# Optimization experiments

Hardware: AMD Instinct MI355X
Metric: run time of the kernel (lower is better)

Reference implementation:

```python
import jax, jax.numpy as jnp
import numpy as np

N = 50000   # nodes
E = 800000  # edges
D = 128     # input feature dim
HID = 64    # hidden dim
NEG_SLOPE = 0.2


def setup_inputs() -> dict:
    key = jax.random.key(0)
    ks = jax.random.split(key, 12)
    s = 0.1
    x = jax.random.normal(ks[0], (N, D), jnp.float32)
    edge_index = jax.random.randint(ks[1], (2, E), 0, N, dtype=jnp.int64)
    # layer 1: GATConv(128 -> 64, heads=2, concat=False)
    W1 = jax.random.normal(ks[2], (D, 2 * HID), jnp.float32) * s
    a_src1 = jax.random.normal(ks[3], (2, HID), jnp.float32) * s
    a_dst1 = jax.random.normal(ks[4], (2, HID), jnp.float32) * s
    b1 = jnp.zeros((HID,), jnp.float32)
    # layer 2: GATConv(64 -> 64, heads=1, concat=False)
    W2 = jax.random.normal(ks[5], (HID, HID), jnp.float32) * s
    a_src2 = jax.random.normal(ks[6], (1, HID), jnp.float32) * s
    a_dst2 = jax.random.normal(ks[7], (1, HID), jnp.float32) * s
    b2 = jnp.zeros((HID,), jnp.float32)
    # classifier Linear(64 -> 2)
    Wc = jax.random.normal(ks[8], (HID, 2), jnp.float32) * s
    bc = jnp.zeros((2,), jnp.float32)
    return {"x": x, "edge_index": edge_index, "W1": W1, "a_src1": a_src1,
            "a_dst1": a_dst1, "b1": b1, "W2": W2, "a_src2": a_src2,
            "a_dst2": a_dst2, "b2": b2, "Wc": Wc, "bc": bc}


def _gat_layer(x, src, dst, W, a_s, a_d, b, n):
    """PyG GATConv (concat=False -> mean over heads), eval mode."""
    H, C = a_s.shape
    h = (x @ W).reshape(n, H, C)                      # [N,H,C]
    alpha_s = jnp.sum(h * a_s, axis=-1)               # [N,H]
    alpha_d = jnp.sum(h * a_d, axis=-1)               # [N,H]
    e = jax.nn.leaky_relu(alpha_s[src] + alpha_d[dst], NEG_SLOPE)  # [E,H]
    # segment softmax over incoming edges of each target node
    m = jax.ops.segment_max(e, dst, num_segments=n)   # [N,H]
    e = jnp.exp(e - m[dst])
    denom = jax.ops.segment_sum(e, dst, num_segments=n)
    alpha = e / (denom[dst] + 1e-16)                  # [E,H]
    msg = h[src] * alpha[:, :, None]                  # [E,H,C]
    out = jax.ops.segment_sum(msg, dst, num_segments=n)  # [N,H,C]
    return out.mean(axis=1) + b                       # [N,C]


def reference(x, edge_index, W1, a_src1, a_dst1, b1, W2, a_src2, a_dst2, b2, Wc, bc):
    n = x.shape[0]
    loops = jnp.arange(n, dtype=edge_index.dtype)     # PyG add_self_loops=True
    src = jnp.concatenate([edge_index[0], loops])
    dst = jnp.concatenate([edge_index[1], loops])
    h = jax.nn.elu(_gat_layer(x, src, dst, W1, a_src1, a_dst1, b1, n))
    h = jax.nn.elu(_gat_layer(h, src, dst, W2, a_src2, a_dst2, b2, n))
    logits = h @ Wc + bc
    return jax.nn.log_softmax(logits, axis=1)
```

## Files before the change

### kernel.cpp

```cpp
#include <hip/hip_runtime.h>
#include <math.h>

#define NN 50000
#define NE 800000
#define NT (NE + NN)
#define SCAN_BLK 1024
#define NSCAN ((NN + SCAN_BLK - 1) / SCAN_BLK)
#define NBUCK 196
#define BE 4096
#define NBLK_B ((NT + BE - 1) / BE)
#define CAP 6144
#define NBLK_G ((NN + 63) / 64)

typedef short bf16x8 __attribute__((ext_vector_type(8)));
typedef float f32x4 __attribute__((ext_vector_type(4)));
union U16x8 { uint4 u; bf16x8 s; };

__device__ __forceinline__ unsigned pk_bf16x2(float x, float y) {
  unsigned ux = __float_as_uint(x); ux = ux + 0x7FFFu + ((ux >> 16) & 1u);
  unsigned uy = __float_as_uint(y); uy = uy + 0x7FFFu + ((uy >> 16) & 1u);
  return (ux >> 16) | (uy & 0xFFFF0000u);
}
__device__ __forceinline__ unsigned short bf16_1(float x) {
  unsigned u = __float_as_uint(x); u = u + 0x7FFFu + ((u >> 16) & 1u);
  return (unsigned short)(u >> 16);
}
__device__ __forceinline__ float blo(unsigned v) { return __uint_as_float(v << 16); }
__device__ __forceinline__ float bhi(unsigned v) { return __uint_as_float(v & 0xFFFF0000u); }

__global__ __launch_bounds__(256) void k_prep(const float* __restrict__ W1, const float* __restrict__ W2,
                                              unsigned short* __restrict__ w1f,
                                              unsigned short* __restrict__ w2f,
                                              int* __restrict__ deg, int* __restrict__ bcur) {
  int i = blockIdx.x * 256 + threadIdx.x;
  if (i < NN) deg[i] = 0;
  if (i < NBUCK) bcur[i] = i * CAP;
  if (i < 128 * 128) {
    int k = i >> 7, col = i & 127;
    int ct = col >> 4, kt = k >> 5, lane = (((k >> 3) & 3) << 4) | (col & 15), j = k & 7;
    w1f[(((ct << 2) | kt) * 64 + lane) * 8 + j] = bf16_1(W1[i]);
  } else if (i < 128 * 128 + 64 * 64) {
    int e = i - 128 * 128;
    int k = e >> 6, col = e & 63;
    int ct = col >> 4, kt = k >> 5, lane = (((k >> 3) & 3) << 4) | (col & 15), j = k & 7;
    w2f[(((ct << 1) | kt) * 64 + lane) * 8 + j] = bf16_1(W2[e]);
  }
}

__global__ __launch_bounds__(256) void k_gb(
    const int* __restrict__ src, const int* __restrict__ dst,
    int* __restrict__ bcur, unsigned* __restrict__ staging, int* __restrict__ deg,
    const float* __restrict__ x, const unsigned short* __restrict__ w1f,
    const float* __restrict__ asw_g, const float* __restrict__ adw_g,
    unsigned short* __restrict__ h1b, float* __restrict__ as1, float* __restrict__ ad1) {
  __shared__ int hist[NBUCK];
  __shared__ int base[NBUCK];
  if (blockIdx.x < NBLK_B) {
    const int t = threadIdx.x;
    const int e0 = blockIdx.x * BE;
    if (t < NBUCK) hist[t] = 0;
    __syncthreads();
    for (int j = t; j < BE; j += 256) {
      int i = e0 + j;
      if (i >= NT) break;
      int d = (i < NE) ? dst[i] : (i - NE);
      atomicAdd(&hist[d >> 8], 1);
      atomicAdd(&deg[d], 1);
    }
    __syncthreads();
    if (t < NBUCK) {
      int c = hist[t];
      base[t] = c ? atomicAdd(&bcur[t], c) : 0;
      hist[t] = 0;
    }
    __syncthreads();
    for (int j = t; j < BE; j += 256) {
      int i = e0 + j;
      if (i >= NT) break;
      int s, d;
      if (i < NE) { s = src[i]; d = dst[i]; } else { s = d = i - NE; }
      int b = d >> 8;
      int off = atomicAdd(&hist[b], 1);
      staging[base[b] + off] = ((unsigned)d << 16) | (unsigned)s;
    }
    return;
  }
  const int bid = blockIdx.x - NBLK_B;
  const int t = threadIdx.x;
  const int wid = t >> 6, l = t & 63;
  const int lr = l & 15, lg = l >> 4;
  const int arow = bid * 64 + wid * 16 + lr;
  const bool aok = arow < NN;

  float asw_t[8], adw_t[8];
#pragma unroll
  for (int ct = 0; ct < 8; ++ct) {
    asw_t[ct] = asw_g[ct * 16 + lr];
    adw_t[ct] = adw_g[ct * 16 + lr];
  }

  f32x4 acc[8];
#pragma unroll
  for (int ct = 0; ct < 8; ++ct) acc[ct] = (f32x4){0.f, 0.f, 0.f, 0.f};

#pragma unroll
  for (int kt = 0; kt < 4; ++kt) {
    U16x8 a;
    if (aok) {
      const float* xp = &x[(long long)arow * 128 + kt * 32 + lg * 8];
      float4 f0 = *(const float4*)xp;
      float4 f1 = *(const float4*)(xp + 4);
      a.u.x = pk_bf16x2(f0.x, f0.y); a.u.y = pk_bf16x2(f0.z, f0.w);
      a.u.z = pk_bf16x2(f1.x, f1.y); a.u.w = pk_bf16x2(f1.z, f1.w);
    } else {
      a.u = make_uint4(0, 0, 0, 0);
    }
#pragma unroll
    for (int ct = 0; ct < 8; ++ct) {
      U16x8 b;
      b.u = *(const uint4*)&w1f[(((ct << 2) | kt) * 64 + l) * 8];
      acc[ct] = __builtin_amdgcn_mfma_f32_16x16x32_bf16(a.s, b.s, acc[ct], 0, 0, 0);
    }
  }

  const int gr0 = bid * 64 + wid * 16 + lg * 4;
#pragma unroll
  for (int reg = 0; reg < 4; ++reg) {
    int grow = gr0 + reg;
    bool ok = grow < NN;
    float s0 = 0.f, s1 = 0.f, d0 = 0.f, d1 = 0.f;
#pragma unroll
    for (int ct = 0; ct < 8; ++ct) {
      float v = acc[ct][reg];
      if (ok) h1b[(long long)grow * 128 + ct * 16 + lr] = bf16_1(v);
      if (ct < 4) { s0 += v * asw_t[ct]; d0 += v * adw_t[ct]; }
      else        { s1 += v * asw_t[ct]; d1 += v * adw_t[ct]; }
    }
#pragma unroll
    for (int off = 1; off < 16; off <<= 1) {
      s0 += __shfl_xor(s0, off); d0 += __shfl_xor(d0, off);
      s1 += __shfl_xor(s1, off); d1 += __shfl_xor(d1, off);
    }
    if (ok && lr == 0) {
      as1[grow * 2] = s0; as1[grow * 2 + 1] = s1;
      ad1[grow * 2] = d0; ad1[grow * 2 + 1] = d1;
    }
  }
}

__global__ __launch_bounds__(SCAN_BLK) void k_scan1(const int* __restrict__ deg,
                                                    int* __restrict__ rowptr, int* __restrict__ part) {
  __shared__ int s[SCAN_BLK];
  int t = threadIdx.x;
  int g = blockIdx.x * SCAN_BLK + t;
  s[t] = (g < NN) ? deg[g] : 0;
  __syncthreads();
  for (int off = 1; off < SCAN_BLK; off <<= 1) {
    int u = (t >= off) ? s[t - off] : 0;
    __syncthreads();
    s[t] += u;
    __syncthreads();
  }
  if (g < NN) rowptr[g + 1] = s[t];
  if (t == SCAN_BLK - 1) part[blockIdx.x] = s[t];
}

__global__ __launch_bounds__(SCAN_BLK) void k_scan3(int* __restrict__ rowptr,
                                                    const int* __restrict__ part) {
  __shared__ int sOff;
  int t = threadIdx.x;
  if (t < 64) {
    int self = (t < NSCAN) ? part[t] : 0;
    int v = self;
#pragma unroll
    for (int off = 1; off < 64; off <<= 1) {
      int u = __shfl_up(v, off);
      if (t >= off) v += u;
    }
    if (t == blockIdx.x) sOff = v - self;
  }
  __syncthreads();
  const int boff = sOff;
  int g = blockIdx.x * SCAN_BLK + t;
  if (g < NN) rowptr[g + 1] += boff;
  if (g == 0) rowptr[0] = 0;
}

__global__ __launch_bounds__(256) void k_scatter2(const unsigned* __restrict__ staging,
                                                  const int* __restrict__ bcur,
                                                  const int* __restrict__ rowptr,
                                                  unsigned short* __restrict__ csr16) {
  __shared__ int lcur[256];
  const int b = blockIdx.x;
  const int t = threadIdx.x;
  int nlo = b << 8, nhi = nlo + 256;
  if (nhi > NN) nhi = NN;
  if (nlo + t < nhi) lcur[t] = rowptr[nlo + t];
  __syncthreads();
  const int s0 = b * CAP;
  const int cnt = bcur[b] - s0;
  for (int k = t; k < cnt; k += 256) {
    unsigned e = staging[s0 + k];
    int d = (int)(e >> 16);
    int pos = atomicAdd(&lcur[d - nlo], 1);
    csr16[pos] = (unsigned short)(e & 0xFFFFu);
  }
}

__global__ __launch_bounds__(256) void k_gat1(
    const int* __restrict__ rowptr, const unsigned short* __restrict__ csr16,
    const unsigned* __restrict__ h1u, const float2* __restrict__ as1,
    const float2* __restrict__ ad1, const float* __restrict__ b1,
    unsigned* __restrict__ out1b) {
  __shared__ float2 sw[4][2][64];
  const int t = threadIdx.x;
  const int wv = t >> 6;
  const int n = blockIdx.x * 4 + wv;
  if (n >= NN) return;
  const int p = t & 63;
  const int h = p >> 5;
  const int beg = rowptr[n], end = rowptr[n + 1];
  const int deg = end - beg;
  const float2 adn = ad1[n];

  float acc0 = 0.f, acc1 = 0.f;
  float inv;

  if (deg <= 64) {
    int s = 0; float e0 = -1e30f, e1 = -1e30f;
    if (p < deg) {
      s = csr16[beg + p];
      float2 a = as1[s];
      e0 = a.x + adn.x; e0 = fmaxf(e0, 0.2f * e0);
      e1 = a.y + adn.y; e1 = fmaxf(e1, 0.2f * e1);
    }
    float m0 = e0, m1 = e1;
#pragma unroll
    for (int off = 1; off < 64; off <<= 1) {
      m0 = fmaxf(m0, __shfl_xor(m0, off));
      m1 = fmaxf(m1, __shfl_xor(m1, off));
    }
    float w0 = (p < deg) ? __expf(e0 - m0) : 0.f;
    float w1 = (p < deg) ? __expf(e1 - m1) : 0.f;
    float d0 = w0, d1 = w1;
#pragma unroll
    for (int off = 1; off < 64; off <<= 1) {
      d0 += __shfl_xor(d0, off);
      d1 += __shfl_xor(d1, off);
    }
    sw[wv][0][p] = make_float2(__int_as_float(s), w0);
    sw[wv][1][p] = make_float2(__int_as_float(s), w1);
    __builtin_amdgcn_wave_barrier();
    inv = 1.f / ((h ? d1 : d0) + 1e-16f);

    int j = 0;
    for (; j + 8 <= deg; j += 8) {
      float2 a[8]; unsigned v[8];
#pragma unroll
      for (int u = 0; u < 8; ++u) a[u] = sw[wv][h][j + u];
#pragma unroll
      for (int u = 0; u < 8; ++u) v[u] = h1u[(__float_as_int(a[u].x) << 6) + p];
#pragma unroll
      for (int u = 0; u < 8; ++u) {
        acc0 += a[u].y * blo(v[u]);
        acc1 += a[u].y * bhi(v[u]);
      }
    }
    if (j + 4 <= deg) {
      float2 a[4]; unsigned v[4];
#pragma unroll
      for (int u = 0; u < 4; ++u) a[u] = sw[wv][h][j + u];
#pragma unroll
      for (int u = 0; u < 4; ++u) v[u] = h1u[(__float_as_int(a[u].x) << 6) + p];
#pragma unroll
      for (int u = 0; u < 4; ++u) {
        acc0 += a[u].y * blo(v[u]);
        acc1 += a[u].y * bhi(v[u]);
      }
      j += 4;
    }
    for (; j < deg; ++j) {
      float2 a = sw[wv][h][j];
      unsigned v = h1u[(__float_as_int(a.x) << 6) + p];
      acc0 += a.y * blo(v); acc1 += a.y * bhi(v);
    }
  } else {
    float m0 = -1e30f, d0 = 0.f, m1 = -1e30f, d1 = 0.f;
    for (int k = beg + p; k < end; k += 64) {
      float2 a = as1[csr16[k]];
      float e0 = a.x + adn.x; e0 = fmaxf(e0, 0.2f * e0);
      float e1 = a.y + adn.y; e1 = fmaxf(e1, 0.2f * e1);
      if (e0 > m0) { d0 *= __expf(m0 - e0); m0 = e0; }
      d0 += __expf(e0 - m0);
      if (e1 > m1) { d1 *= __expf(m1 - e1); m1 = e1; }
      d1 += __expf(e1 - m1);
    }
#pragma unroll
    for (int off = 1; off < 64; off <<= 1) {
      float mo = __shfl_xor(m0, off), dd = __shfl_xor(d0, off);
      float mn = fmaxf(m0, mo);
      d0 = d0 * __expf(m0 - mn) + dd * __expf(mo - mn);
      m0 = mn;
      mo = __shfl_xor(m1, off); dd = __shfl_xor(d1, off);
      mn = fmaxf(m1, mo);
      d1 = d1 * __expf(m1 - mn) + dd * __expf(mo - mn);
      m1 = mn;
    }
    inv = 1.f / ((h ? d1 : d0) + 1e-16f);
    for (int c0 = beg; c0 < end; c0 += 64) {
      int nc = end - c0; if (nc > 64) nc = 64;
      int s = 0; float w0 = 0.f, w1 = 0.f;
      if (p < nc) {
        s = csr16[c0 + p];
        float2 a = as1[s];
        float e0 = a.x + adn.x; e0 = fmaxf(e0, 0.2f * e0);
        float e1 = a.y + adn.y; e1 = fmaxf(e1, 0.2f * e1);
        w0 = __expf(e0 - m0);
        w1 = __expf(e1 - m1);
      }
      __builtin_amdgcn_wave_barrier();
      sw[wv][0][p] = make_float2(__int_as_float(s), w0);
      sw[wv][1][p] = make_float2(__int_as_float(s), w1);
      __builtin_amdgcn_wave_barrier();
      for (int j = 0; j < nc; ++j) {
        float2 a = sw[wv][h][j];
        unsigned v = h1u[(__float_as_int(a.x) << 6) + p];
        acc0 += a.y * blo(v); acc1 += a.y * bhi(v);
      }
      __builtin_amdgcn_wave_barrier();
    }
  }

  acc0 *= inv; acc1 *= inv;
  acc0 += __shfl_xor(acc0, 32);
  acc1 += __shfl_xor(acc1, 32);
  if (p < 32) {
    float u0 = 0.5f * acc0 + b1[2 * p];
    float u1 = 0.5f * acc1 + b1[2 * p + 1];
    u0 = u0 > 0.f ? u0 : expm1f(u0);
    u1 = u1 > 0.f ? u1 : expm1f(u1);
    out1b[n * 32 + p] = pk_bf16x2(u0, u1);
  }
}

__global__ __launch_bounds__(256) void k_gemm2(
    const unsigned short* __restrict__ in_b, const unsigned short* __restrict__ w2f,
    const float* __restrict__ asw_g, const float* __restrict__ adw_g,
    unsigned short* __restrict__ h2b, float* __restrict__ as2, float* __restrict__ ad2) {
  const int t = threadIdx.x;
  const int wid = t >> 6, l = t & 63;
  const int lr = l & 15, lg = l >> 4;
  const int arow = blockIdx.x * 64 + wid * 16 + lr;
  const bool aok = arow < NN;

  float asw_t[4], adw_t[4];
#pragma unroll
  for (int ct = 0; ct < 4; ++ct) {
    asw_t[ct] = asw_g[ct * 16 + lr];
    adw_t[ct] = adw_g[ct * 16 + lr];
  }

  f32x4 acc[4];
#pragma unroll
  for (int ct = 0; ct < 4; ++ct) acc[ct] = (f32x4){0.f, 0.f, 0.f, 0.f};

#pragma unroll
  for (int kt = 0; kt < 2; ++kt) {
    U16x8 a;
    if (aok) a.u = *(const uint4*)&in_b[(long long)arow * 64 + kt * 32 + lg * 8];
    else a.u = make_uint4(0, 0, 0, 0);
#pragma unroll
    for (int ct = 0; ct < 4; ++ct) {
      U16x8 b;
      b.u = *(const uint4*)&w2f[(((ct << 1) | kt) * 64 + l) * 8];
      acc[ct] = __builtin_amdgcn_mfma_f32_16x16x32_bf16(a.s, b.s, acc[ct], 0, 0, 0);
    }
  }

  const int gr0 = blockIdx.x * 64 + wid * 16 + lg * 4;
#pragma unroll
  for (int reg = 0; reg < 4; ++reg) {
    int grow = gr0 + reg;
    bool ok = grow < NN;
    float s0 = 0.f, d0 = 0.f;
#pragma unroll
    for (int ct = 0; ct < 4; ++ct) {
      float v = acc[ct][reg];
      if (ok) h2b[(long long)grow * 64 + ct * 16 + lr] = bf16_1(v);
      s0 += v * asw_t[ct]; d0 += v * adw_t[ct];
    }
#pragma unroll
    for (int off = 1; off < 16; off <<= 1) {
      s0 += __shfl_xor(s0, off); d0 += __shfl_xor(d0, off);
    }
    if (ok && lr == 0) { as2[grow] = s0; ad2[grow] = d0; }
  }
}

__global__ __launch_bounds__(256) void k_gat2(
    const int* __restrict__ rowptr, const unsigned short* __restrict__ csr16,
    const unsigned* __restrict__ h2u, const float* __restrict__ as2,
    const float* __restrict__ ad2, const float* __restrict__ b2,
    const float* __restrict__ Wc, const float* __restrict__ bc,
    float* __restrict__ out) {
  __shared__ float2 sw[4][64];
  const int t = threadIdx.x;
  const int wv = t >> 6;
  const int n = blockIdx.x * 4 + wv;
  if (n >= NN) return;
  const int p = t & 63;
  const int half = p >> 5;
  const int q = p & 31;
  const int beg = rowptr[n], end = rowptr[n + 1];
  const int deg = end - beg;
  const float adn = ad2[n];

  float acc0 = 0.f, acc1 = 0.f;
  float inv;

  if (deg <= 64) {
    int s = 0; float e = -1e30f;
    if (p < deg) {
      s = csr16[beg + p];
      e = as2[s] + adn;
      e = fmaxf(e, 0.2f * e);
    }
    float m = e;
#pragma unroll
    for (int off = 1; off < 64; off <<= 1) m = fmaxf(m, __shfl_xor(m, off));
    float w = (p < deg) ? __expf(e - m) : 0.f;
    float d = w;
#pragma unroll
    for (int off = 1; off < 64; off <<= 1) d += __shfl_xor(d, off);
    sw[wv][p] = make_float2(__int_as_float(s), w);
    __builtin_amdgcn_wave_barrier();
    inv = 1.f / (d + 1e-16f);

    int niter = (deg + 1) >> 1;
    int i = 0;
    for (; i + 4 <= niter; i += 4) {
      float2 a[4]; unsigned v[4];
#pragma unroll
      for (int u = 0; u < 4; ++u) a[u] = sw[wv][2 * (i + u) + half];
#pragma unroll
      for (int u = 0; u < 4; ++u) v[u] = h2u[(__float_as_int(a[u].x) << 5) + q];
#pragma unroll
      for (int u = 0; u < 4; ++u) {
        acc0 += a[u].y * blo(v[u]);
        acc1 += a[u].y * bhi(v[u]);
      }
    }
    if (i + 2 <= niter) {
      float2 a0 = sw[wv][2 * i + half];
      float2 a1 = sw[wv][2 * (i + 1) + half];
      unsigned v0 = h2u[(__float_as_int(a0.x) << 5) + q];
      unsigned v1 = h2u[(__float_as_int(a1.x) << 5) + q];
      acc0 += a0.y * blo(v0); acc1 += a0.y * bhi(v0);
      acc0 += a1.y * blo(v1); acc1 += a1.y * bhi(v1);
      i += 2;
    }
    if (i < niter) {
      float2 a = sw[wv][2 * i + half];
      unsigned v = h2u[(__float_as_int(a.x) << 5) + q];
      acc0 += a.y * blo(v); acc1 += a.y * bhi(v);
    }
  } else {
    float m = -1e30f, d = 0.f;
    for (int k = beg + p; k < end; k += 64) {
      float e = as2[csr16[k]] + adn;
      e = fmaxf(e, 0.2f * e);
      if (e > m) { d *= __expf(m - e); m = e; }
      d += __expf(e - m);
    }
#pragma unroll
    for (int off = 1; off < 64; off <<= 1) {
      float mo = __shfl_xor(m, off), dd = __shfl_xor(d, off);
      float mn = fmaxf(m, mo);
      d = d * __expf(m - mn) + dd * __expf(mo - mn);
      m = mn;
    }
    inv = 1.f / (d + 1e-16f);
    for (int c0 = beg; c0 < end; c0 += 64) {
      int nc = end - c0; if (nc > 64) nc = 64;
      int s = 0; float w = 0.f;
      if (p < nc) {
        s = csr16[c0 + p];
        float e = as2[s] + adn;
        e = fmaxf(e, 0.2f * e);
        w = __expf(e - m);
      }
      __builtin_amdgcn_wave_barrier();
      sw[wv][p] = make_float2(__int_as_float(s), w);
      __builtin_amdgcn_wave_barrier();
      int niter = (nc + 1) >> 1;
      for (int i = 0; i < niter; ++i) {
        int j = 2 * i + half;
        float2 a = sw[wv][j < nc ? j : 0];
        float wj = (j < nc) ? a.y : 0.f;
        unsigned v = h2u[(__float_as_int(a.x) << 5) + q];
        acc0 += wj * blo(v); acc1 += wj * bhi(v);
      }
      __builtin_amdgcn_wave_barrier();
    }
  }

  acc0 += __shfl_xor(acc0, 32);
  acc1 += __shfl_xor(acc1, 32);
  float v0 = acc0 * inv + b2[2 * q];
  float v1 = acc1 * inv + b2[2 * q + 1];
  v0 = v0 > 0.f ? v0 : expm1f(v0);
  v1 = v1 > 0.f ? v1 : expm1f(v1);
  float l0 = v0 * Wc[4 * q] + v1 * Wc[4 * q + 2];
  float l1 = v0 * Wc[4 * q + 1] + v1 * Wc[4 * q + 3];
#pragma unroll
  for (int off = 1; off < 32; off <<= 1) {
    l0 += __shfl_xor(l0, off);
    l1 += __shfl_xor(l1, off);
  }
  if (p == 0) {
    l0 += bc[0]; l1 += bc[1];
    float mx = fmaxf(l0, l1);
    float lse = mx + logf(expf(l0 - mx) + expf(l1 - mx));
    out[n * 2] = l0 - lse;
    out[n * 2 + 1] = l1 - lse;
  }
}

extern "C" void kernel_launch(void* const* d_in, const int* in_sizes, int n_in,
                              void* d_out, int out_size, void* d_ws, size_t ws_size,
                              hipStream_t stream) {
  const float* x    = (const float*)d_in[0];
  const int*   ei   = (const int*)d_in[1];
  const float* W1   = (const float*)d_in[2];
  const float* as1w = (const float*)d_in[3];
  const float* ad1w = (const float*)d_in[4];
  const float* b1   = (const float*)d_in[5];
  const float* W2   = (const float*)d_in[6];
  const float* as2w = (const float*)d_in[7];
  const float* ad2w = (const float*)d_in[8];
  const float* b2   = (const float*)d_in[9];
  const float* Wc   = (const float*)d_in[10];
  const float* bc   = (const float*)d_in[11];
  float* out = (float*)d_out;

  const int* src = ei;
  const int* dst = ei + NE;

  char* p = (char*)d_ws;
  unsigned short* h1b = (unsigned short*)p; p += sizeof(unsigned short) * (long long)NN * 128;
  unsigned short* out1b = (unsigned short*)p; p += sizeof(unsigned short) * (long long)NN * 64;
  unsigned short* h2b = (unsigned short*)p; p += sizeof(unsigned short) * (long long)NN * 64;
  float* as1  = (float*)p; p += sizeof(float) * NN * 2;
  float* ad1  = (float*)p; p += sizeof(float) * NN * 2;
  float* as2  = (float*)p; p += sizeof(float) * NN;
  float* ad2  = (float*)p; p += sizeof(float) * NN;
  int* deg     = (int*)p; p += sizeof(int) * NN;
  int* rowptr  = (int*)p; p += sizeof(int) * (NN + 1);
  int* part    = (int*)p; p += sizeof(int) * ((NSCAN + 63) & ~63);
  int* bcur    = (int*)p; p += sizeof(int) * ((NBUCK + 63) & ~63);
  unsigned* staging = (unsigned*)p; p += sizeof(unsigned) * (long long)NBUCK * CAP;
  unsigned short* csr16 = (unsigned short*)p; p += sizeof(unsigned short) * (long long)NT;
  unsigned short* w1f = (unsigned short*)p; p += sizeof(unsigned short) * 128 * 128;
  unsigned short* w2f = (unsigned short*)p; p += sizeof(unsigned short) * 64 * 64;

  k_prep<<<(NN + 255) / 256, 256, 0, stream>>>(W1, W2, w1f, w2f, deg, bcur);
  k_gb<<<NBLK_B + NBLK_G, 256, 0, stream>>>(src, dst, bcur, staging, deg,
                                            x, w1f, as1w, ad1w, h1b, as1, ad1);
  k_scan1<<<NSCAN, SCAN_BLK, 0, stream>>>(deg, rowptr, part);
  k_scan3<<<NSCAN, SCAN_BLK, 0, stream>>>(rowptr, part);
  k_scatter2<<<NBUCK, 256, 0, stream>>>(staging, bcur, rowptr, csr16);

  k_gat1<<<(NN + 3) / 4, 256, 0, stream>>>(rowptr, csr16, (const unsigned*)h1b,
                                           (const float2*)as1, (const float2*)ad1, b1,
                                           (unsigned*)out1b);

  k_gemm2<<<(NN + 63) / 64, 256, 0, stream>>>(out1b, w2f, as2w, ad2w, h2b, as2, ad2);
  k_gat2<<<(NN + 3) / 4, 256, 0, stream>>>(rowptr, csr16, (const unsigned*)h2b,
                                           as2, ad2, b2, Wc, bc, out);
}
```

Baseline: 142.7 us.

## Derive CSR row pointers from bucket counts, dropping global degree atomics and scans

Drops the per-edge global degree atomics and the two-kernel 50k-element prefix scan. A single-block scan over the 196 bucket counts now gives each bucket's base offset. The scatter kernel builds a per-node histogram in shared memory and scans it locally to write rowptr. This removes 850k global atomics and one kernel launch, at the cost of a second pass over each bucket's staging data in the scatter kernel.

```diff
diff --git a/kernel.cpp b/kernel.cpp
--- a/kernel.cpp
+++ b/kernel.cpp
@@ -4,8 +4,6 @@
 #define NN 50000
 #define NE 800000
 #define NT (NE + NN)
-#define SCAN_BLK 1024
-#define NSCAN ((NN + SCAN_BLK - 1) / SCAN_BLK)
 #define NBUCK 196
 #define BE 4096
 #define NBLK_B ((NT + BE - 1) / BE)
@@ -31,9 +29,8 @@
 __global__ __launch_bounds__(256) void k_prep(const float* __restrict__ W1, const float* __restrict__ W2,
                                               unsigned short* __restrict__ w1f,
                                               unsigned short* __restrict__ w2f,
-                                              int* __restrict__ deg, int* __restrict__ bcur) {
+                                              int* __restrict__ bcur) {
   int i = blockIdx.x * 256 + threadIdx.x;
-  if (i < NN) deg[i] = 0;
   if (i < NBUCK) bcur[i] = i * CAP;
   if (i < 128 * 128) {
     int k = i >> 7, col = i & 127;
@@ -49,7 +46,7 @@
 
 __global__ __launch_bounds__(256) void k_gb(
     const int* __restrict__ src, const int* __restrict__ dst,
-    int* __restrict__ bcur, unsigned* __restrict__ staging, int* __restrict__ deg,
+    int* __restrict__ bcur, unsigned* __restrict__ staging,
     const float* __restrict__ x, const unsigned short* __restrict__ w1f,
     const float* __restrict__ asw_g, const float* __restrict__ adw_g,
     unsigned short* __restrict__ h1b, float* __restrict__ as1, float* __restrict__ ad1) {
@@ -65,7 +62,6 @@
       if (i >= NT) break;
       int d = (i < NE) ? dst[i] : (i - NE);
       atomicAdd(&hist[d >> 8], 1);
-      atomicAdd(&deg[d], 1);
     }
     __syncthreads();
     if (t < NBUCK) {
@@ -148,61 +144,65 @@
   }
 }
 
-__global__ __launch_bounds__(SCAN_BLK) void k_scan1(const int* __restrict__ deg,
-                                                    int* __restrict__ rowptr, int* __restrict__ part) {
-  __shared__ int s[SCAN_BLK];
-  int t = threadIdx.x;
-  int g = blockIdx.x * SCAN_BLK + t;
-  s[t] = (g < NN) ? deg[g] : 0;
+__global__ __launch_bounds__(256) void k_bscan(const int* __restrict__ bcur, int* __restrict__ bbase) {
+  __shared__ int wsum[4];
+  const int t = threadIdx.x;
+  const int l = t & 63, w = t >> 6;
+  int v = (t < NBUCK) ? bcur[t] - t * CAP : 0;
+  int sc = v;
+#pragma unroll
+  for (int off = 1; off < 64; off <<= 1) {
+    int u = __shfl_up(sc, off);
+    if (l >= off) sc += u;
+  }
+  if (l == 63) wsum[w] = sc;
   __syncthreads();
-  for (int off = 1; off < SCAN_BLK; off <<= 1) {
-    int u = (t >= off) ? s[t - off] : 0;
-    __syncthreads();
-    s[t] += u;
-    __syncthreads();
-  }
-  if (g < NN) rowptr[g + 1] = s[t];
-  if (t == SCAN_BLK - 1) part[blockIdx.x] = s[t];
-}
-
-__global__ __launch_bounds__(SCAN_BLK) void k_scan3(int* __restrict__ rowptr,
-                                                    const int* __restrict__ part) {
-  __shared__ int sOff;
-  int t = threadIdx.x;
-  if (t < 64) {
-    int self = (t < NSCAN) ? part[t] : 0;
-    int v = self;
-#pragma unroll
-    for (int off = 1; off < 64; off <<= 1) {
-      int u = __shfl_up(v, off);
-      if (t >= off) v += u;
-    }
-    if (t == blockIdx.x) sOff = v - self;
-  }
-  __syncthreads();
-  const int boff = sOff;
-  int g = blockIdx.x * SCAN_BLK + t;
-  if (g < NN) rowptr[g + 1] += boff;
-  if (g == 0) rowptr[0] = 0;
+  int wo = 0;
+  for (int i = 0; i < w; ++i) wo += wsum[i];
+  int incl = sc + wo;
+  if (t < NBUCK) bbase[t] = incl - v;
+  if (t == 255) bbase[NBUCK] = incl;
 }
 
 __global__ __launch_bounds__(256) void k_scatter2(const unsigned* __restrict__ staging,
                                                   const int* __restrict__ bcur,
-                                                  const int* __restrict__ rowptr,
+                                                  const int* __restrict__ bbase,
+                                                  int* __restrict__ rowptr,
                                                   unsigned short* __restrict__ csr16) {
-  __shared__ int lcur[256];
+  __shared__ int lcnt[256];
+  __shared__ int wsum[4];
   const int b = blockIdx.x;
   const int t = threadIdx.x;
-  int nlo = b << 8, nhi = nlo + 256;
-  if (nhi > NN) nhi = NN;
-  if (nlo + t < nhi) lcur[t] = rowptr[nlo + t];
+  const int nlo = b << 8;
+  lcnt[t] = 0;
   __syncthreads();
   const int s0 = b * CAP;
   const int cnt = bcur[b] - s0;
+  for (int k = t; k < cnt; k += 256)
+    atomicAdd(&lcnt[(int)(staging[s0 + k] >> 16) - nlo], 1);
+  __syncthreads();
+  int v = lcnt[t];
+  int sc = v;
+  const int l = t & 63, w = t >> 6;
+#pragma unroll
+  for (int off = 1; off < 64; off <<= 1) {
+    int u = __shfl_up(sc, off);
+    if (l >= off) sc += u;
+  }
+  if (l == 63) wsum[w] = sc;
+  __syncthreads();
+  int wo = 0;
+  for (int i = 0; i < w; ++i) wo += wsum[i];
+  const int base = bbase[b] + sc + wo - v;
+  if (nlo + t < NN) rowptr[nlo + t] = base;
+  if (b == NBUCK - 1 && t == 0) rowptr[NN] = bbase[NBUCK];
+  __syncthreads();
+  lcnt[t] = base;
+  __syncthreads();
   for (int k = t; k < cnt; k += 256) {
     unsigned e = staging[s0 + k];
-    int d = (int)(e >> 16);
-    int pos = atomicAdd(&lcur[d - nlo], 1);
+    int d = (int)(e >> 16) - nlo;
+    int pos = atomicAdd(&lcnt[d], 1);
     csr16[pos] = (unsigned short)(e & 0xFFFFu);
   }
 }
@@ -554,21 +554,19 @@
   float* ad1  = (float*)p; p += sizeof(float) * NN * 2;
   float* as2  = (float*)p; p += sizeof(float) * NN;
   float* ad2  = (float*)p; p += sizeof(float) * NN;
-  int* deg     = (int*)p; p += sizeof(int) * NN;
-  int* rowptr  = (int*)p; p += sizeof(int) * (NN + 1);
-  int* part    = (int*)p; p += sizeof(int) * ((NSCAN + 63) & ~63);
+  int* rowptr  = (int*)p; p += sizeof(int) * (NN + 64);
   int* bcur    = (int*)p; p += sizeof(int) * ((NBUCK + 63) & ~63);
+  int* bbase   = (int*)p; p += sizeof(int) * ((NBUCK + 64) & ~63);
   unsigned* staging = (unsigned*)p; p += sizeof(unsigned) * (long long)NBUCK * CAP;
   unsigned short* csr16 = (unsigned short*)p; p += sizeof(unsigned short) * (long long)NT;
   unsigned short* w1f = (unsigned short*)p; p += sizeof(unsigned short) * 128 * 128;
   unsigned short* w2f = (unsigned short*)p; p += sizeof(unsigned short) * 64 * 64;
 
-  k_prep<<<(NN + 255) / 256, 256, 0, stream>>>(W1, W2, w1f, w2f, deg, bcur);
-  k_gb<<<NBLK_B + NBLK_G, 256, 0, stream>>>(src, dst, bcur, staging, deg,
+  k_prep<<<(128 * 128 + 64 * 64 + 255) / 256, 256, 0, stream>>>(W1, W2, w1f, w2f, bcur);
+  k_gb<<<NBLK_B + NBLK_G, 256, 0, stream>>>(src, dst, bcur, staging,
                                             x, w1f, as1w, ad1w, h1b, as1, ad1);
-  k_scan1<<<NSCAN, SCAN_BLK, 0, stream>>>(deg, rowptr, part);
-  k_scan3<<<NSCAN, SCAN_BLK, 0, stream>>>(rowptr, part);
-  k_scatter2<<<NBUCK, 256, 0, stream>>>(staging, bcur, rowptr, csr16);
+  k_bscan<<<1, 256, 0, stream>>>(bcur, bbase);
+  k_scatter2<<<NBUCK, 256, 0, stream>>>(staging, bcur, bbase, rowptr, csr16);
 
   k_gat1<<<(NN + 3) / 4, 256, 0, stream>>>(rowptr, csr16, (const unsigned*)h1b,
                                            (const float2*)as1, (const float2*)ad1, b1,
```

After: 116.1 us. -18.6%, faster.
